# Performance work log

Hardware: AMD Instinct MI355X
Metric: run time of the kernel (lower is better)

Reference implementation:

```python
import jax, jax.numpy as jnp
import numpy as np

BATCH, N_VERTS, N_FACES, CUT_NUM, N_SAMPLES, C = 4, 10000, 20000, 8, 80000, 128


def setup_inputs() -> dict:
    key = jax.random.key(0)
    k1, k2, k3, k4, k5 = jax.random.split(key, 5)
    x_features = jax.random.normal(k1, (BATCH, N_VERTS, C), dtype=jnp.float32)
    B = jax.random.uniform(k2, (BATCH, N_SAMPLES, 3), dtype=jnp.float32)
    x_graph = jax.random.randint(k3, (N_VERTS, CUT_NUM), 0, N_SAMPLES, dtype=jnp.int32)
    F = jax.random.randint(k4, (N_FACES, 3), 0, N_VERTS, dtype=jnp.int32)
    I = jax.random.randint(k5, (N_SAMPLES,), 0, N_FACES, dtype=jnp.int32)
    return {"x_features": x_features, "B": B, "x_graph": x_graph, "F": F, "I": I}


def reference(x_features, B, x_graph, F, I):
    # mapping_face_Xid: [S, 3] vertex ids of the face each resample point lies on
    mapping_face_Xid = F[I]
    # gather per-vertex features for the 3 face corners: [b, S, 3, C]
    mapping_face_Xfeature = x_features[:, mapping_face_Xid]
    # barycentric interpolation (weighted sum over 3 corners): [b, S, C]
    N_x_features = jnp.einsum('bsjc,bsj->bsc', mapping_face_Xfeature, B)
    # gather resampled disk points per vertex and subtract center feature:
    # [b, V, cut_num, C] - [b, V, 1, C]
    x_disk_features = N_x_features[:, x_graph] - x_features[:, :, None, :]
    return x_disk_features
```

## Files before the change

kernel.cpp:

```cpp
#include <hip/hip_runtime.h>

#define BATCH   4
#define N_VERTS 10000
#define N_FACES 20000
#define CUT_NUM 8
#define N_SAMP  80000
#define CC      128
#define NXCD    8

typedef float          f32x4 __attribute__((ext_vector_type(4)));
typedef int            i32x4 __attribute__((ext_vector_type(4)));
typedef unsigned short u16x4 __attribute__((ext_vector_type(4)));
typedef unsigned short u16x8 __attribute__((ext_vector_type(8)));

#define XB16_BYTES ((size_t)BATCH * N_VERTS * CC * 2)
#define QUAD_BYTES ((size_t)N_VERTS * CUT_NUM * sizeof(i32x4))
#define CONV_BLOCKS 2500
#define IDX_BLOCKS  313

__device__ inline float bf16_to_f32(unsigned short u) {
    return __uint_as_float((unsigned)u << 16);
}

__device__ inline unsigned short f32_to_bf16(float f) {
    unsigned u = __float_as_uint(f);
    unsigned rounding = 0x7fffu + ((u >> 16) & 1u);
    return (unsigned short)((u + rounding) >> 16);
}

__global__ __launch_bounds__(256) void prep_kernel(
    const float* __restrict__ xf,
    const int*   __restrict__ xg,
    const int*   __restrict__ Fc,
    const int*   __restrict__ Iv,
    unsigned short* __restrict__ x16,
    i32x4*          __restrict__ quad)
{
    const int bid = blockIdx.x;
    if (bid < CONV_BLOCKS) {
        const size_t i = ((size_t)bid * 256 + threadIdx.x) * 8;
        const f32x4 a = *(const f32x4*)(xf + i);
        const f32x4 b = *(const f32x4*)(xf + i + 4);
        u16x8 o;
        o.s0 = f32_to_bf16(a.x); o.s1 = f32_to_bf16(a.y);
        o.s2 = f32_to_bf16(a.z); o.s3 = f32_to_bf16(a.w);
        o.s4 = f32_to_bf16(b.x); o.s5 = f32_to_bf16(b.y);
        o.s6 = f32_to_bf16(b.z); o.s7 = f32_to_bf16(b.w);
        *(u16x8*)(x16 + i) = o;
    } else {
        const int e = (bid - CONV_BLOCKS) * 256 + threadIdx.x;
        if (e < N_VERTS * CUT_NUM) {
            const int s   = xg[e];
            const int fid = Iv[s];
            i32x4 q;
            q.x = Fc[fid * 3 + 0];
            q.y = Fc[fid * 3 + 1];
            q.z = Fc[fid * 3 + 2];
            q.w = s;
            quad[e] = q;
        }
    }
}

__global__ __launch_bounds__(256) void disk_features_main(
    const unsigned short* __restrict__ x16,
    const float*          __restrict__ Bw,
    const i32x4*          __restrict__ quad,
    float*                __restrict__ out)
{
    const int L    = blockIdx.x;
    const int xcd  = L & (NXCD - 1);
    const int b    = xcd >> 1;
    const int vp   = (L >> 3) + (xcd & 1) * (N_VERTS / 4);
    const int t    = threadIdx.x;
    const int g    = t >> 4;
    const int lane = t & 15;
    const int k    = g & 7;
    const int v    = vp * 2 + (g >> 3);
    const int c0   = lane * 8;

    const i32x4 q = quad[v * CUT_NUM + k];

    const float* bw = Bw + ((size_t)b * N_SAMP + q.w) * 3;
    const float w0 = bw[0];
    const float w1 = bw[1];
    const float w2 = bw[2];

    const unsigned short* xb = x16 + (size_t)b * N_VERTS * CC;
    const u16x8 a0 = *(const u16x8*)(xb + (size_t)q.x * CC + c0);
    const u16x8 a1 = *(const u16x8*)(xb + (size_t)q.y * CC + c0);
    const u16x8 a2 = *(const u16x8*)(xb + (size_t)q.z * CC + c0);
    const u16x8 ax = *(const u16x8*)(xb + (size_t)v   * CC + c0);

    f32x4 r0, r1;
    #pragma unroll
    for (int j = 0; j < 4; ++j) {
        const float f0 = bf16_to_f32(a0[j]);
        const float f1 = bf16_to_f32(a1[j]);
        const float f2 = bf16_to_f32(a2[j]);
        const float fx = bf16_to_f32(ax[j]);
        r0[j] = fmaf(w0, f0, fmaf(w1, f1, fmaf(w2, f2, -fx)));
    }
    #pragma unroll
    for (int j = 0; j < 4; ++j) {
        const float f0 = bf16_to_f32(a0[j + 4]);
        const float f1 = bf16_to_f32(a1[j + 4]);
        const float f2 = bf16_to_f32(a2[j + 4]);
        const float fx = bf16_to_f32(ax[j + 4]);
        r1[j] = fmaf(w0, f0, fmaf(w1, f1, fmaf(w2, f2, -fx)));
    }

    float* dst = out + ((((size_t)b * N_VERTS + v) * CUT_NUM + k) * CC + c0);
    __builtin_nontemporal_store(r0, (f32x4*)dst);
    __builtin_nontemporal_store(r1, (f32x4*)(dst + 4));
}

__global__ __launch_bounds__(256) void idx_prep(
    const int* __restrict__ xg,
    const int* __restrict__ Fc,
    const int* __restrict__ Iv,
    i32x4*     __restrict__ quad)
{
    const int e = blockIdx.x * 256 + threadIdx.x;
    if (e >= N_VERTS * CUT_NUM) return;
    const int s   = xg[e];
    const int fid = Iv[s];
    i32x4 q;
    q.x = Fc[fid * 3 + 0];
    q.y = Fc[fid * 3 + 1];
    q.z = Fc[fid * 3 + 2];
    q.w = s;
    quad[e] = q;
}

__global__ __launch_bounds__(256) void disk_features_f32(
    const float* __restrict__ xf,
    const float* __restrict__ Bw,
    const i32x4* __restrict__ quad,
    float*       __restrict__ out)
{
    const int v    = blockIdx.x;
    const int b    = blockIdx.y;
    const int t    = threadIdx.x;
    const int k    = t >> 5;
    const int lane = t & 31;
    const int c0   = lane * 4;

    const i32x4 q = quad[v * CUT_NUM + k];

    const float* bw = Bw + ((size_t)b * N_SAMP + q.w) * 3;
    const float w0 = bw[0];
    const float w1 = bw[1];
    const float w2 = bw[2];

    const float* xb = xf + (size_t)b * N_VERTS * CC;
    const f32x4 f0 = *(const f32x4*)(xb + (size_t)q.x * CC + c0);
    const f32x4 f1 = *(const f32x4*)(xb + (size_t)q.y * CC + c0);
    const f32x4 f2 = *(const f32x4*)(xb + (size_t)q.z * CC + c0);
    const f32x4 fx = *(const f32x4*)(xb + (size_t)v   * CC + c0);

    f32x4 r;
    r.x = fmaf(w0, f0.x, fmaf(w1, f1.x, fmaf(w2, f2.x, -fx.x)));
    r.y = fmaf(w0, f0.y, fmaf(w1, f1.y, fmaf(w2, f2.y, -fx.y)));
    r.z = fmaf(w0, f0.z, fmaf(w1, f1.z, fmaf(w2, f2.z, -fx.z)));
    r.w = fmaf(w0, f0.w, fmaf(w1, f1.w, fmaf(w2, f2.w, -fx.w)));

    f32x4* dst = (f32x4*)(out + ((((size_t)b * N_VERTS + v) * CUT_NUM + k) * CC + c0));
    __builtin_nontemporal_store(r, dst);
}

__global__ __launch_bounds__(256) void fused_disk_features(
    const float* __restrict__ xf,
    const float* __restrict__ Bw,
    const int*   __restrict__ xg,
    const int*   __restrict__ Fc,
    const int*   __restrict__ Iv,
    float*       __restrict__ out)
{
    const int v    = blockIdx.x;
    const int b    = blockIdx.y;
    const int t    = threadIdx.x;
    const int k    = t >> 5;
    const int lane = t & 31;
    const int c0   = lane * 4;

    const int s   = xg[v * CUT_NUM + k];
    const int fid = Iv[s];
    const int v0  = Fc[fid * 3 + 0];
    const int v1  = Fc[fid * 3 + 1];
    const int v2  = Fc[fid * 3 + 2];

    const float* bw = Bw + ((size_t)b * N_SAMP + s) * 3;
    const float w0 = bw[0];
    const float w1 = bw[1];
    const float w2 = bw[2];

    const float* xb = xf + (size_t)b * N_VERTS * CC;
    const f32x4 f0 = *(const f32x4*)(xb + (size_t)v0 * CC + c0);
    const f32x4 f1 = *(const f32x4*)(xb + (size_t)v1 * CC + c0);
    const f32x4 f2 = *(const f32x4*)(xb + (size_t)v2 * CC + c0);
    const f32x4 fx = *(const f32x4*)(xb + (size_t)v  * CC + c0);

    f32x4 r;
    r.x = fmaf(w0, f0.x, fmaf(w1, f1.x, fmaf(w2, f2.x, -fx.x)));
    r.y = fmaf(w0, f0.y, fmaf(w1, f1.y, fmaf(w2, f2.y, -fx.y)));
    r.z = fmaf(w0, f0.z, fmaf(w1, f1.z, fmaf(w2, f2.z, -fx.z)));
    r.w = fmaf(w0, f0.w, fmaf(w1, f1.w, fmaf(w2, f2.w, -fx.w)));

    f32x4* dst = (f32x4*)(out + ((((size_t)b * N_VERTS + v) * CUT_NUM + k) * CC + c0));
    __builtin_nontemporal_store(r, dst);
}

extern "C" void kernel_launch(void* const* d_in, const int* in_sizes, int n_in,
                              void* d_out, int out_size, void* d_ws, size_t ws_size,
                              hipStream_t stream) {
    const float* xf = (const float*)d_in[0];
    const float* Bw = (const float*)d_in[1];
    const int*   xg = (const int*)  d_in[2];
    const int*   Fc = (const int*)  d_in[3];
    const int*   Iv = (const int*)  d_in[4];
    float*       out = (float*)d_out;

    const int n_e = N_VERTS * CUT_NUM;

    if (ws_size >= XB16_BYTES + QUAD_BYTES) {
        unsigned short* x16  = (unsigned short*)d_ws;
        i32x4*          quad = (i32x4*)((char*)d_ws + XB16_BYTES);
        prep_kernel<<<CONV_BLOCKS + IDX_BLOCKS, 256, 0, stream>>>(xf, xg, Fc, Iv, x16, quad);
        disk_features_main<<<N_VERTS * BATCH / 2, 256, 0, stream>>>(x16, Bw, quad, out);
    } else if (ws_size >= QUAD_BYTES) {
        i32x4* quad = (i32x4*)d_ws;
        idx_prep<<<(n_e + 255) / 256, 256, 0, stream>>>(xg, Fc, Iv, quad);
        dim3 grid(N_VERTS, BATCH);
        disk_features_f32<<<grid, 256, 0, stream>>>(xf, Bw, quad, out);
    } else {
        dim3 grid(N_VERTS, BATCH);
        fused_disk_features<<<grid, 256, 0, stream>>>(xf, Bw, xg, Fc, Iv, out);
    }
}
```

Before: 47.35 us.

## Loop over cut points per thread and precompute per-batch barycentric weight records

The main kernel now gives each 16-lane group one vertex and loops over all 8 cut neighbours. The centre-vertex feature is loaded once and reused, rather than loaded once per cut point. The prep kernel gains a third block range that gathers the barycentric weights for each (edge, batch) into padded float4 records, so the main kernel does one coalesced 16-byte load instead of three scattered loads from B. This costs an extra workspace buffer, more prep work, fewer blocks in the main kernel (2504), and a serial dependent loop per thread that may reduce memory-level parallelism.

```diff
diff --git a/kernel.cpp b/kernel.cpp
--- a/kernel.cpp
+++ b/kernel.cpp
@@ -10,13 +10,15 @@
 
 typedef float          f32x4 __attribute__((ext_vector_type(4)));
 typedef int            i32x4 __attribute__((ext_vector_type(4)));
-typedef unsigned short u16x4 __attribute__((ext_vector_type(4)));
 typedef unsigned short u16x8 __attribute__((ext_vector_type(8)));
 
+#define N_E        (N_VERTS * CUT_NUM)
 #define XB16_BYTES ((size_t)BATCH * N_VERTS * CC * 2)
-#define QUAD_BYTES ((size_t)N_VERTS * CUT_NUM * sizeof(i32x4))
+#define QUAD_BYTES ((size_t)N_E * sizeof(i32x4))
+#define WREC_BYTES ((size_t)N_E * BATCH * sizeof(f32x4))
 #define CONV_BLOCKS 2500
 #define IDX_BLOCKS  313
+#define WREC_BLOCKS 1250
 
 __device__ inline float bf16_to_f32(unsigned short u) {
     return __uint_as_float((unsigned)u << 16);
@@ -30,11 +32,13 @@
 
 __global__ __launch_bounds__(256) void prep_kernel(
     const float* __restrict__ xf,
+    const float* __restrict__ Bw,
     const int*   __restrict__ xg,
     const int*   __restrict__ Fc,
     const int*   __restrict__ Iv,
     unsigned short* __restrict__ x16,
-    i32x4*          __restrict__ quad)
+    i32x4*          __restrict__ quad,
+    f32x4*          __restrict__ wrec)
 {
     const int bid = blockIdx.x;
     if (bid < CONV_BLOCKS) {
@@ -47,9 +51,9 @@
         o.s4 = f32_to_bf16(b.x); o.s5 = f32_to_bf16(b.y);
         o.s6 = f32_to_bf16(b.z); o.s7 = f32_to_bf16(b.w);
         *(u16x8*)(x16 + i) = o;
-    } else {
+    } else if (bid < CONV_BLOCKS + IDX_BLOCKS) {
         const int e = (bid - CONV_BLOCKS) * 256 + threadIdx.x;
-        if (e < N_VERTS * CUT_NUM) {
+        if (e < N_E) {
             const int s   = xg[e];
             const int fid = Iv[s];
             i32x4 q;
@@ -59,10 +63,110 @@
             q.w = s;
             quad[e] = q;
         }
+    } else {
+        const int i = (bid - CONV_BLOCKS - IDX_BLOCKS) * 256 + threadIdx.x;
+        if (i < N_E * BATCH) {
+            const int e = i >> 2;
+            const int b = i & 3;
+            const int s = xg[e];
+            const float* p = Bw + ((size_t)b * N_SAMP + s) * 3;
+            f32x4 w;
+            w.x = p[0]; w.y = p[1]; w.z = p[2]; w.w = 0.0f;
+            wrec[i] = w;
+        }
     }
 }
 
 __global__ __launch_bounds__(256) void disk_features_main(
+    const unsigned short* __restrict__ x16,
+    const f32x4*          __restrict__ wrec,
+    const i32x4*          __restrict__ quad,
+    float*                __restrict__ out)
+{
+    const int L    = blockIdx.x;
+    const int xcd  = L & (NXCD - 1);
+    const int b    = xcd >> 1;
+    const int half = xcd & 1;
+    const int idx  = L >> 3;
+    const int chunk = idx + half * 313;
+    if (chunk >= 625) return;
+
+    const int t    = threadIdx.x;
+    const int g    = t >> 4;
+    const int lane = t & 15;
+    const int c0   = lane * 8;
+    const int v    = chunk * 16 + g;
+
+    const unsigned short* xb = x16 + (size_t)b * N_VERTS * CC;
+
+    const u16x8 axv = *(const u16x8*)(xb + (size_t)v * CC + c0);
+    float fx[8];
+    #pragma unroll
+    for (int j = 0; j < 8; ++j) fx[j] = bf16_to_f32(axv[j]);
+
+    const int e0 = v * CUT_NUM;
+    float* dstv = out + ((size_t)b * N_VERTS + v) * CUT_NUM * CC + c0;
+
+    #pragma unroll
+    for (int k = 0; k < CUT_NUM; ++k) {
+        const i32x4 q = quad[e0 + k];
+        const f32x4 w = wrec[(size_t)(e0 + k) * 4 + b];
+        const u16x8 a0 = *(const u16x8*)(xb + (size_t)q.x * CC + c0);
+        const u16x8 a1 = *(const u16x8*)(xb + (size_t)q.y * CC + c0);
+        const u16x8 a2 = *(const u16x8*)(xb + (size_t)q.z * CC + c0);
+
+        f32x4 r0, r1;
+        #pragma unroll
+        for (int j = 0; j < 4; ++j)
+            r0[j] = fmaf(w.x, bf16_to_f32(a0[j]),
+                    fmaf(w.y, bf16_to_f32(a1[j]),
+                    fmaf(w.z, bf16_to_f32(a2[j]), -fx[j])));
+        #pragma unroll
+        for (int j = 0; j < 4; ++j)
+            r1[j] = fmaf(w.x, bf16_to_f32(a0[j + 4]),
+                    fmaf(w.y, bf16_to_f32(a1[j + 4]),
+                    fmaf(w.z, bf16_to_f32(a2[j + 4]), -fx[j + 4])));
+
+        float* dst = dstv + (size_t)k * CC;
+        __builtin_nontemporal_store(r0, (f32x4*)dst);
+        __builtin_nontemporal_store(r1, (f32x4*)(dst + 4));
+    }
+}
+
+__global__ __launch_bounds__(256) void idx_prep(
+    const int* __restrict__ xg,
+    const int* __restrict__ Fc,
+    const int* __restrict__ Iv,
+    i32x4*     __restrict__ quad)
+{
+    const int e = blockIdx.x * 256 + threadIdx.x;
+    if (e >= N_E) return;
+    const int s   = xg[e];
+    const int fid = Iv[s];
+    i32x4 q;
+    q.x = Fc[fid * 3 + 0];
+    q.y = Fc[fid * 3 + 1];
+    q.z = Fc[fid * 3 + 2];
+    q.w = s;
+    quad[e] = q;
+}
+
+__global__ __launch_bounds__(256) void to_bf16_kernel(
+    const float* __restrict__ xf, unsigned short* __restrict__ x16)
+{
+    const size_t i = ((size_t)blockIdx.x * 256 + threadIdx.x) * 8;
+    if (i >= (size_t)BATCH * N_VERTS * CC) return;
+    const f32x4 a = *(const f32x4*)(xf + i);
+    const f32x4 b = *(const f32x4*)(xf + i + 4);
+    u16x8 o;
+    o.s0 = f32_to_bf16(a.x); o.s1 = f32_to_bf16(a.y);
+    o.s2 = f32_to_bf16(a.z); o.s3 = f32_to_bf16(a.w);
+    o.s4 = f32_to_bf16(b.x); o.s5 = f32_to_bf16(b.y);
+    o.s6 = f32_to_bf16(b.z); o.s7 = f32_to_bf16(b.w);
+    *(u16x8*)(x16 + i) = o;
+}
+
+__global__ __launch_bounds__(256) void disk_features_r11(
     const unsigned short* __restrict__ x16,
     const float*          __restrict__ Bw,
     const i32x4*          __restrict__ quad,
@@ -94,79 +198,19 @@
 
     f32x4 r0, r1;
     #pragma unroll
-    for (int j = 0; j < 4; ++j) {
-        const float f0 = bf16_to_f32(a0[j]);
-        const float f1 = bf16_to_f32(a1[j]);
-        const float f2 = bf16_to_f32(a2[j]);
-        const float fx = bf16_to_f32(ax[j]);
-        r0[j] = fmaf(w0, f0, fmaf(w1, f1, fmaf(w2, f2, -fx)));
-    }
-    #pragma unroll
-    for (int j = 0; j < 4; ++j) {
-        const float f0 = bf16_to_f32(a0[j + 4]);
-        const float f1 = bf16_to_f32(a1[j + 4]);
-        const float f2 = bf16_to_f32(a2[j + 4]);
-        const float fx = bf16_to_f32(ax[j + 4]);
-        r1[j] = fmaf(w0, f0, fmaf(w1, f1, fmaf(w2, f2, -fx)));
-    }
+    for (int j = 0; j < 4; ++j)
+        r0[j] = fmaf(w0, bf16_to_f32(a0[j]),
+                fmaf(w1, bf16_to_f32(a1[j]),
+                fmaf(w2, bf16_to_f32(a2[j]), -bf16_to_f32(ax[j]))));
+    #pragma unroll
+    for (int j = 0; j < 4; ++j)
+        r1[j] = fmaf(w0, bf16_to_f32(a0[j + 4]),
+                fmaf(w1, bf16_to_f32(a1[j + 4]),
+                fmaf(w2, bf16_to_f32(a2[j + 4]), -bf16_to_f32(ax[j + 4]))));
 
     float* dst = out + ((((size_t)b * N_VERTS + v) * CUT_NUM + k) * CC + c0);
     __builtin_nontemporal_store(r0, (f32x4*)dst);
     __builtin_nontemporal_store(r1, (f32x4*)(dst + 4));
-}
-
-__global__ __launch_bounds__(256) void idx_prep(
-    const int* __restrict__ xg,
-    const int* __restrict__ Fc,
-    const int* __restrict__ Iv,
-    i32x4*     __restrict__ quad)
-{
-    const int e = blockIdx.x * 256 + threadIdx.x;
-    if (e >= N_VERTS * CUT_NUM) return;
-    const int s   = xg[e];
-    const int fid = Iv[s];
-    i32x4 q;
-    q.x = Fc[fid * 3 + 0];
-    q.y = Fc[fid * 3 + 1];
-    q.z = Fc[fid * 3 + 2];
-    q.w = s;
-    quad[e] = q;
-}
-
-__global__ __launch_bounds__(256) void disk_features_f32(
-    const float* __restrict__ xf,
-    const float* __restrict__ Bw,
-    const i32x4* __restrict__ quad,
-    float*       __restrict__ out)
-{
-    const int v    = blockIdx.x;
-    const int b    = blockIdx.y;
-    const int t    = threadIdx.x;
-    const int k    = t >> 5;
-    const int lane = t & 31;
-    const int c0   = lane * 4;
-
-    const i32x4 q = quad[v * CUT_NUM + k];
-
-    const float* bw = Bw + ((size_t)b * N_SAMP + q.w) * 3;
-    const float w0 = bw[0];
-    const float w1 = bw[1];
-    const float w2 = bw[2];
-
-    const float* xb = xf + (size_t)b * N_VERTS * CC;
-    const f32x4 f0 = *(const f32x4*)(xb + (size_t)q.x * CC + c0);
-    const f32x4 f1 = *(const f32x4*)(xb + (size_t)q.y * CC + c0);
-    const f32x4 f2 = *(const f32x4*)(xb + (size_t)q.z * CC + c0);
-    const f32x4 fx = *(const f32x4*)(xb + (size_t)v   * CC + c0);
-
-    f32x4 r;
-    r.x = fmaf(w0, f0.x, fmaf(w1, f1.x, fmaf(w2, f2.x, -fx.x)));
-    r.y = fmaf(w0, f0.y, fmaf(w1, f1.y, fmaf(w2, f2.y, -fx.y)));
-    r.z = fmaf(w0, f0.z, fmaf(w1, f1.z, fmaf(w2, f2.z, -fx.z)));
-    r.w = fmaf(w0, f0.w, fmaf(w1, f1.w, fmaf(w2, f2.w, -fx.w)));
-
-    f32x4* dst = (f32x4*)(out + ((((size_t)b * N_VERTS + v) * CUT_NUM + k) * CC + c0));
-    __builtin_nontemporal_store(r, dst);
 }
 
 __global__ __launch_bounds__(256) void fused_disk_features(
@@ -221,18 +265,19 @@
     const int*   Iv = (const int*)  d_in[4];
     float*       out = (float*)d_out;
 
-    const int n_e = N_VERTS * CUT_NUM;
-
-    if (ws_size >= XB16_BYTES + QUAD_BYTES) {
+    if (ws_size >= XB16_BYTES + QUAD_BYTES + WREC_BYTES) {
         unsigned short* x16  = (unsigned short*)d_ws;
         i32x4*          quad = (i32x4*)((char*)d_ws + XB16_BYTES);
-        prep_kernel<<<CONV_BLOCKS + IDX_BLOCKS, 256, 0, stream>>>(xf, xg, Fc, Iv, x16, quad);
-        disk_features_main<<<N_VERTS * BATCH / 2, 256, 0, stream>>>(x16, Bw, quad, out);
-    } else if (ws_size >= QUAD_BYTES) {
-        i32x4* quad = (i32x4*)d_ws;
-        idx_prep<<<(n_e + 255) / 256, 256, 0, stream>>>(xg, Fc, Iv, quad);
-        dim3 grid(N_VERTS, BATCH);
-        disk_features_f32<<<grid, 256, 0, stream>>>(xf, Bw, quad, out);
+        f32x4*          wrec = (f32x4*)((char*)d_ws + XB16_BYTES + QUAD_BYTES);
+        prep_kernel<<<CONV_BLOCKS + IDX_BLOCKS + WREC_BLOCKS, 256, 0, stream>>>(
+            xf, Bw, xg, Fc, Iv, x16, quad, wrec);
+        disk_features_main<<<2504, 256, 0, stream>>>(x16, wrec, quad, out);
+    } else if (ws_size >= XB16_BYTES + QUAD_BYTES) {
+        unsigned short* x16  = (unsigned short*)d_ws;
+        i32x4*          quad = (i32x4*)((char*)d_ws + XB16_BYTES);
+        to_bf16_kernel<<<CONV_BLOCKS, 256, 0, stream>>>(xf, x16);
+        idx_prep<<<IDX_BLOCKS, 256, 0, stream>>>(xg, Fc, Iv, quad);
+        disk_features_r11<<<N_VERTS * BATCH / 2, 256, 0, stream>>>(x16, Bw, quad, out);
     } else {
         dim3 grid(N_VERTS, BATCH);
         fused_disk_features<<<grid, 256, 0, stream>>>(xf, Bw, xg, Fc, Iv, out);
```

Measured after the change: 56.65 us. +19.6%, slower.
